# Kernel tuning notes

Measured on AMD Instinct MI355X. Metric: run time of the kernel, lower is better.

The kernel has to match this reference:

```python
import jax, jax.numpy as jnp
import numpy as np


def setup_inputs() -> dict:
    key = jax.random.key(0)
    k1, k2, k3 = jax.random.split(key, 3)
    B, L, S, H, E, D = 2, 512, 512, 8, 32, 64
    queries = jax.random.normal(k1, (B, L, H, E), dtype=jnp.float32)
    keys = jax.random.normal(k2, (B, S, H, E), dtype=jnp.float32)
    values = jax.random.normal(k3, (B, S, H, D), dtype=jnp.float32)
    v = jnp.ones((E,), dtype=jnp.float32)
    attn_mask_add = jnp.zeros((L, S), dtype=jnp.float32)
    key_lengths_add = jnp.zeros((B, S), dtype=jnp.float32)
    return {
        "queries": queries,
        "keys": keys,
        "values": values,
        "v": v,
        "attn_mask_add": attn_mask_add,
        "key_lengths_add": key_lengths_add,
    }


def reference(queries, keys, values, v, attn_mask_add, key_lengths_add):
    # Additive (Bahdanau) attention.
    # queries: (B,L,H,E), keys: (B,S,H,E), values: (B,S,H,D)
    # Broadcast add -> tanh -> contract with v: (B,L,S,H,E) -> (B,H,L,S)
    feat = jnp.tanh(queries[:, :, None, :, :] + keys[:, None, :, :, :])  # (B,L,S,H,E)
    scores = jnp.einsum("blshe,e->bhls", feat, v)  # (B,H,L,S)
    scores = scores + attn_mask_add[None, None, :, :]          # (L,S) attn mask
    scores = scores + key_lengths_add[:, None, None, :]        # (B,S) key-length mask
    A = jax.nn.softmax(scores, axis=-1)  # (B,H,L,S); dropout is identity (p=0 / eval)
    V = jnp.einsum("bhls,bshd->blhd", A, values)  # (B,L,H,D)
    return V
```

## Files before the change

kernel.cpp:

```cpp
#include <hip/hip_runtime.h>


#define BB 2
#define LL 512
#define SS 512
#define HH 8
#define EE 32
#define DD 64

#define WS_EK_OFF 0
#define WS_EQ_OFF (2u * 1024u * 1024u)
#define WS_VT_OFF (4u * 1024u * 1024u)
#define WS_PR_OFF (8u * 1024u * 1024u)
#define WS_SM_OFF (16u * 1024u * 1024u)

typedef __attribute__((ext_vector_type(8))) short bf16x8;
typedef __attribute__((ext_vector_type(4))) float f32x4;
typedef __attribute__((ext_vector_type(4))) unsigned u32x4;

__device__ __forceinline__ unsigned short f2bf(float f) {
    unsigned u = __float_as_uint(f);
    u += 0x7FFFu + ((u >> 16) & 1u);
    return (unsigned short)(u >> 16);
}
__device__ __forceinline__ float fast_exp2(float x) {
#if __has_builtin(__builtin_amdgcn_exp2f)
    return __builtin_amdgcn_exp2f(x);
#else
    return exp2f(x);
#endif
}
__device__ __forceinline__ float fast_rcp(float x) {
    return __builtin_amdgcn_rcpf(x);
}
__device__ __forceinline__ float bcastf(float x) {
    return __int_as_float(__builtin_amdgcn_readfirstlane(__float_as_int(x)));
}

#define SCV 2.885390081777927f

__global__ __launch_bounds__(256) void prep_kernel(
    const float* __restrict__ q, const float* __restrict__ k,
    const float* __restrict__ vals, float* __restrict__ ws)
{
    unsigned gid = blockIdx.x * 256 + threadIdx.x;
    if (gid < 32768u) {
        unsigned i  = gid;
        unsigned s  = i & 511u;
        unsigned e8 = (i >> 9) & 3u;
        unsigned h  = (i >> 11) & 7u;
        unsigned b  = i >> 14;
        const float* kr = k + (((size_t)b * SS + s) * HH + h) * EE + e8 * 8;
        float4 k0 = *(const float4*)kr;
        float4 k1 = *(const float4*)(kr + 4);
        u32x4 pk;
        pk[0] = (unsigned)f2bf(fast_exp2(SCV * k0.x)) |
                ((unsigned)f2bf(fast_exp2(SCV * k0.y)) << 16);
        pk[1] = (unsigned)f2bf(fast_exp2(SCV * k0.z)) |
                ((unsigned)f2bf(fast_exp2(SCV * k0.w)) << 16);
        pk[2] = (unsigned)f2bf(fast_exp2(SCV * k1.x)) |
                ((unsigned)f2bf(fast_exp2(SCV * k1.y)) << 16);
        pk[3] = (unsigned)f2bf(fast_exp2(SCV * k1.z)) |
                ((unsigned)f2bf(fast_exp2(SCV * k1.w)) << 16);
        ((u32x4*)((char*)ws + WS_EK_OFF))[i] = pk;
    } else if (gid < 98304u) {
        unsigned i = gid - 32768u;
        float4 qv = ((const float4*)q)[i];
        float4 ev = make_float4(fast_exp2(SCV * qv.x), fast_exp2(SCV * qv.y),
                                fast_exp2(SCV * qv.z), fast_exp2(SCV * qv.w));
        ((float4*)(ws + WS_EQ_OFF / 4))[i] = ev;
    } else {
        unsigned i      = gid - 98304u;
        unsigned lane   = i & 63u;
        unsigned c      = (i >> 6) & 15u;
        unsigned dchunk = (i >> 10) & 3u;
        unsigned h      = (i >> 12) & 7u;
        unsigned b      = i >> 15;
        unsigned qd = lane >> 4, n = lane & 15;
        unsigned d  = dchunk * 16 + n;
        unsigned s0 = c * 32 + qd * 8;
        const float* vb = vals + (((size_t)b * SS + s0) * HH + h) * DD + d;
        u32x4 pk;
        #pragma unroll
        for (int j2 = 0; j2 < 4; j2++) {
            float f0 = vb[(size_t)(2 * j2) * (HH * DD)];
            float f1 = vb[(size_t)(2 * j2 + 1) * (HH * DD)];
            pk[j2] = (unsigned)f2bf(f0) | ((unsigned)f2bf(f1) << 16);
        }
        ((u32x4*)((char*)ws + WS_VT_OFF))[i] = pk;
    }
}

__global__ __launch_bounds__(256) void score_kernel(
    const u32x4* __restrict__ ws_ekb,
    const float* __restrict__ ws_eqf,
    const float* __restrict__ vvec,
    const float* __restrict__ mask,
    const float* __restrict__ klen,
    unsigned short* __restrict__ ws_prob,
    float* __restrict__ ws_sum)
{
    __shared__ u32x4 sek[4 * SS];

    const int tid  = threadIdx.x;
    const int w    = tid >> 6;
    const int lane = tid & 63;
    const int bh   = blockIdx.x >> 6;
    const int lblk = blockIdx.x & 63;
    const int b    = bh >> 3;
    const int h    = bh & 7;
    const int lw   = lblk * 8 + 2 * w;

    {
        const u32x4* esrc = ws_ekb + (size_t)bh * (4 * SS);
        #pragma unroll
        for (int t = 0; t < 8; t++)
            sek[tid + t * 256] = esrc[tid + t * 256];
    }

    float eq0[EE], eq1[EE], v2s[EE];
    {
        const float* q0 = ws_eqf + (((size_t)b * LL + lw) * HH + h) * EE;
        const float* q1 = q0 + HH * EE;
        #pragma unroll
        for (int e = 0; e < EE; e += 4) {
            float4 t0 = *(const float4*)(q0 + e);
            float4 t1 = *(const float4*)(q1 + e);
            eq0[e] = bcastf(t0.x); eq0[e+1] = bcastf(t0.y);
            eq0[e+2] = bcastf(t0.z); eq0[e+3] = bcastf(t0.w);
            eq1[e] = bcastf(t1.x); eq1[e+1] = bcastf(t1.y);
            eq1[e+2] = bcastf(t1.z); eq1[e+3] = bcastf(t1.w);
        }
        const float4* vr = (const float4*)vvec;
        #pragma unroll
        for (int e4 = 0; e4 < EE / 4; e4++) {
            float4 t = vr[e4];
            v2s[e4*4]   = bcastf(-2.f * t.x); v2s[e4*4+1] = bcastf(-2.f * t.y);
            v2s[e4*4+2] = bcastf(-2.f * t.z); v2s[e4*4+3] = bcastf(-2.f * t.w);
        }
    }
    __syncthreads();

    float sc0[SS / 64], sc1[SS / 64];
    for (int i = 0; i < SS / 64; i++) {
        const int s = lane + i * 64;
        u32x4 g0 = sek[s];
        u32x4 g1 = sek[SS + s];
        u32x4 g2 = sek[2 * SS + s];
        u32x4 g3 = sek[3 * SS + s];
        float a0A = 0.f, a0B = 0.f, a1A = 0.f, a1B = 0.f;
        #define PAIR2(u, le, A0, A1)                                          \
        {                                                                     \
            float eklo = __uint_as_float((u) << 16);                          \
            float ekhi = __uint_as_float((u) & 0xffff0000u);                  \
            float qa0 = __builtin_fmaf(eq0[le], eklo, 1.f);                   \
            float qb0 = __builtin_fmaf(eq0[(le) + 1], ekhi, 1.f);             \
            float nm0 = __builtin_fmaf(v2s[le], qb0, v2s[(le) + 1] * qa0);    \
            A0 = __builtin_fmaf(nm0, fast_rcp(qa0 * qb0), A0);                \
            float qa1 = __builtin_fmaf(eq1[le], eklo, 1.f);                   \
            float qb1 = __builtin_fmaf(eq1[(le) + 1], ekhi, 1.f);             \
            float nm1 = __builtin_fmaf(v2s[le], qb1, v2s[(le) + 1] * qa1);    \
            A1 = __builtin_fmaf(nm1, fast_rcp(qa1 * qb1), A1);                \
        }
        PAIR2(g0[0], 0, a0A, a1A)  PAIR2(g0[1], 2, a0B, a1B)
        PAIR2(g0[2], 4, a0A, a1A)  PAIR2(g0[3], 6, a0B, a1B)
        PAIR2(g1[0], 8, a0A, a1A)  PAIR2(g1[1], 10, a0B, a1B)
        PAIR2(g1[2], 12, a0A, a1A) PAIR2(g1[3], 14, a0B, a1B)
        PAIR2(g2[0], 16, a0A, a1A) PAIR2(g2[1], 18, a0B, a1B)
        PAIR2(g2[2], 20, a0A, a1A) PAIR2(g2[3], 22, a0B, a1B)
        PAIR2(g3[0], 24, a0A, a1A) PAIR2(g3[1], 26, a0B, a1B)
        PAIR2(g3[2], 28, a0A, a1A) PAIR2(g3[3], 30, a0B, a1B)
        #undef PAIR2
        sc0[i] = a0A + a0B;
        sc1[i] = a1A + a1B;
    }

    {
        const float* kl = klen + (size_t)b * SS;
        float klv[SS / 64];
        #pragma unroll
        for (int i = 0; i < SS / 64; i++) klv[i] = kl[lane + i * 64];

        #pragma unroll
        for (int r = 0; r < 2; r++) {
            float* sc = r ? sc1 : sc0;
            const float* mrow = mask + (size_t)(lw + r) * SS;
            float ssum = 0.f;
            #pragma unroll
            for (int i = 0; i < SS / 64; i++) {
                float v = fminf(sc[i] + mrow[lane + i * 64] + klv[i], 80.f);
                sc[i] = __expf(v);
                ssum += sc[i];
            }
            #pragma unroll
            for (int off = 1; off < 64; off <<= 1) ssum += __shfl_xor(ssum, off, 64);
            unsigned short* pr = ws_prob + ((size_t)bh * LL + lw + r) * SS;
            #pragma unroll
            for (int i = 0; i < SS / 64; i++)
                pr[lane + i * 64] = f2bf(sc[i]);
            if (lane == 0) ws_sum[(size_t)bh * LL + lw + r] = ssum;
        }
    }
}

__global__ __launch_bounds__(256) void pv_kernel(
    const unsigned short* __restrict__ ws_prob,
    const float* __restrict__ ws_sum,
    const bf16x8* __restrict__ ws_vtf,
    float* __restrict__ out)
{
    const int tid  = threadIdx.x;
    const int w    = tid >> 6;
    const int lane = tid & 63;
    const int bh   = blockIdx.x >> 5;
    const int lt   = blockIdx.x & 31;
    const int b    = bh >> 3;
    const int h    = bh & 7;
    const int l0   = lt * 16;

    const int am = lane & 15;
    const int qd = lane >> 4;
    const unsigned short* ap = ws_prob + ((size_t)bh * LL + l0 + am) * SS + qd * 8;
    const bf16x8* vf = ws_vtf + ((size_t)(bh * 4 + w) * 16) * 64 + lane;

    f32x4 acc = {0.f, 0.f, 0.f, 0.f};
    bf16x8 af[4], bv[4];
    #pragma unroll
    for (int c = 0; c < 4; c++) {
        af[c] = *(const bf16x8*)(ap + c * 32);
        bv[c] = vf[c * 64];
    }
    #pragma unroll
    for (int c = 0; c < SS / 32; c++) {
        acc = __builtin_amdgcn_mfma_f32_16x16x32_bf16(af[c & 3], bv[c & 3],
                                                      acc, 0, 0, 0);
        if (c + 4 < SS / 32) {
            af[c & 3] = *(const bf16x8*)(ap + (c + 4) * 32);
            bv[c & 3] = vf[(c + 4) * 64];
        }
    }
    const int dof = w * 16 + am;
    float* orow = out + (((size_t)b * LL + l0 + qd * 4) * HH + h) * DD + dof;
    const float* sm = ws_sum + (size_t)bh * LL + l0 + qd * 4;
    #pragma unroll
    for (int r = 0; r < 4; r++)
        orow[(size_t)r * (HH * DD)] = acc[r] * fast_rcp(sm[r]);
}

extern "C" void kernel_launch(void* const* d_in, const int* in_sizes, int n_in,
                              void* d_out, int out_size, void* d_ws, size_t ws_size,
                              hipStream_t stream) {
    const float* q    = (const float*)d_in[0];
    const float* k    = (const float*)d_in[1];
    const float* vals = (const float*)d_in[2];
    const float* vvec = (const float*)d_in[3];
    const float* mask = (const float*)d_in[4];
    const float* klen = (const float*)d_in[5];
    float* outp = (float*)d_out;

    float* ws = (float*)d_ws;
    prep_kernel<<<dim3(640), dim3(256), 0, stream>>>(q, k, vals, ws);

    const u32x4* ws_ekb = (const u32x4*)((char*)d_ws + WS_EK_OFF);
    const float* ws_eqf = (const float*)((char*)d_ws + WS_EQ_OFF);
    const bf16x8* ws_vtf = (const bf16x8*)((char*)d_ws + WS_VT_OFF);
    unsigned short* ws_prob = (unsigned short*)((char*)d_ws + WS_PR_OFF);
    float* ws_sum = (float*)((char*)d_ws + WS_SM_OFF);

    score_kernel<<<dim3(BB * HH * (LL / 8)), dim3(256), 0, stream>>>(
        ws_ekb, ws_eqf, vvec, mask, klen, ws_prob, ws_sum);

    pv_kernel<<<dim3(BB * HH * (LL / 16)), dim3(256), 0, stream>>>(
        ws_prob, ws_sum, ws_vtf, outp);
}
```

Baseline: 108.1 us.

## Fuse score and PV kernels via LDS probability tile, compute exp(q) inline

```diff
diff --git a/kernel.cpp b/kernel.cpp
--- a/kernel.cpp
+++ b/kernel.cpp
@@ -9,10 +9,7 @@
 #define DD 64
 
 #define WS_EK_OFF 0
-#define WS_EQ_OFF (2u * 1024u * 1024u)
 #define WS_VT_OFF (4u * 1024u * 1024u)
-#define WS_PR_OFF (8u * 1024u * 1024u)
-#define WS_SM_OFF (16u * 1024u * 1024u)
 
 typedef __attribute__((ext_vector_type(8))) short bf16x8;
 typedef __attribute__((ext_vector_type(4))) float f32x4;
@@ -40,8 +37,8 @@
 #define SCV 2.885390081777927f
 
 __global__ __launch_bounds__(256) void prep_kernel(
-    const float* __restrict__ q, const float* __restrict__ k,
-    const float* __restrict__ vals, float* __restrict__ ws)
+    const float* __restrict__ k, const float* __restrict__ vals,
+    float* __restrict__ ws)
 {
     unsigned gid = blockIdx.x * 256 + threadIdx.x;
     if (gid < 32768u) {
@@ -63,14 +60,8 @@
         pk[3] = (unsigned)f2bf(fast_exp2(SCV * k1.z)) |
                 ((unsigned)f2bf(fast_exp2(SCV * k1.w)) << 16);
         ((u32x4*)((char*)ws + WS_EK_OFF))[i] = pk;
-    } else if (gid < 98304u) {
-        unsigned i = gid - 32768u;
-        float4 qv = ((const float4*)q)[i];
-        float4 ev = make_float4(fast_exp2(SCV * qv.x), fast_exp2(SCV * qv.y),
-                                fast_exp2(SCV * qv.z), fast_exp2(SCV * qv.w));
-        ((float4*)(ws + WS_EQ_OFF / 4))[i] = ev;
     } else {
-        unsigned i      = gid - 98304u;
+        unsigned i      = gid - 32768u;
         unsigned lane   = i & 63u;
         unsigned c      = (i >> 6) & 15u;
         unsigned dchunk = (i >> 10) & 3u;
@@ -91,16 +82,17 @@
     }
 }
 
-__global__ __launch_bounds__(256) void score_kernel(
+__global__ __launch_bounds__(256) void addattn_kernel(
     const u32x4* __restrict__ ws_ekb,
-    const float* __restrict__ ws_eqf,
+    const bf16x8* __restrict__ ws_vtf,
+    const float* __restrict__ q,
     const float* __restrict__ vvec,
     const float* __restrict__ mask,
     const float* __restrict__ klen,
-    unsigned short* __restrict__ ws_prob,
-    float* __restrict__ ws_sum)
+    float* __restrict__ out)
 {
     __shared__ u32x4 sek[4 * SS];
+    __shared__ unsigned short sAb[8][SS];
 
     const int tid  = threadIdx.x;
     const int w    = tid >> 6;
@@ -109,7 +101,8 @@
     const int lblk = blockIdx.x & 63;
     const int b    = bh >> 3;
     const int h    = bh & 7;
-    const int lw   = lblk * 8 + 2 * w;
+    const int l0   = lblk * 8;
+    const int lw   = l0 + 2 * w;
 
     {
         const u32x4* esrc = ws_ekb + (size_t)bh * (4 * SS);
@@ -120,16 +113,20 @@
 
     float eq0[EE], eq1[EE], v2s[EE];
     {
-        const float* q0 = ws_eqf + (((size_t)b * LL + lw) * HH + h) * EE;
+        const float* q0 = q + (((size_t)b * LL + lw) * HH + h) * EE;
         const float* q1 = q0 + HH * EE;
         #pragma unroll
         for (int e = 0; e < EE; e += 4) {
             float4 t0 = *(const float4*)(q0 + e);
             float4 t1 = *(const float4*)(q1 + e);
-            eq0[e] = bcastf(t0.x); eq0[e+1] = bcastf(t0.y);
-            eq0[e+2] = bcastf(t0.z); eq0[e+3] = bcastf(t0.w);
-            eq1[e] = bcastf(t1.x); eq1[e+1] = bcastf(t1.y);
-            eq1[e+2] = bcastf(t1.z); eq1[e+3] = bcastf(t1.w);
+            eq0[e]   = bcastf(fast_exp2(SCV * t0.x));
+            eq0[e+1] = bcastf(fast_exp2(SCV * t0.y));
+            eq0[e+2] = bcastf(fast_exp2(SCV * t0.z));
+            eq0[e+3] = bcastf(fast_exp2(SCV * t0.w));
+            eq1[e]   = bcastf(fast_exp2(SCV * t1.x));
+            eq1[e+1] = bcastf(fast_exp2(SCV * t1.y));
+            eq1[e+2] = bcastf(fast_exp2(SCV * t1.z));
+            eq1[e+3] = bcastf(fast_exp2(SCV * t1.w));
         }
         const float4* vr = (const float4*)vvec;
         #pragma unroll
@@ -194,57 +191,43 @@
             }
             #pragma unroll
             for (int off = 1; off < 64; off <<= 1) ssum += __shfl_xor(ssum, off, 64);
-            unsigned short* pr = ws_prob + ((size_t)bh * LL + lw + r) * SS;
+            float inv = fast_rcp(ssum);
+            const int row = 2 * w + r;
+            const int fsw = (row * 5) & 7;
             #pragma unroll
-            for (int i = 0; i < SS / 64; i++)
-                pr[lane + i * 64] = f2bf(sc[i]);
-            if (lane == 0) ws_sum[(size_t)bh * LL + lw + r] = ssum;
-        }
-    }
-}
-
-__global__ __launch_bounds__(256) void pv_kernel(
-    const unsigned short* __restrict__ ws_prob,
-    const float* __restrict__ ws_sum,
-    const bf16x8* __restrict__ ws_vtf,
-    float* __restrict__ out)
-{
-    const int tid  = threadIdx.x;
-    const int w    = tid >> 6;
-    const int lane = tid & 63;
-    const int bh   = blockIdx.x >> 5;
-    const int lt   = blockIdx.x & 31;
-    const int b    = bh >> 3;
-    const int h    = bh & 7;
-    const int l0   = lt * 16;
-
-    const int am = lane & 15;
-    const int qd = lane >> 4;
-    const unsigned short* ap = ws_prob + ((size_t)bh * LL + l0 + am) * SS + qd * 8;
-    const bf16x8* vf = ws_vtf + ((size_t)(bh * 4 + w) * 16) * 64 + lane;
-
+            for (int i = 0; i < SS / 64; i++) {
+                int col = lane + i * 64;
+                int pos = (((col >> 3) ^ fsw) << 3) | (col & 7);
+                sAb[row][pos] = f2bf(sc[i] * inv);
+            }
+        }
+    }
+    __syncthreads();
+
+    const int am  = lane & 15;
+    const int qd  = lane >> 4;
+    const int dof = w * 16 + am;
+    const int fam = (am * 5) & 7;
+    const bf16x8* vf =
+        ws_vtf + ((size_t)((b * HH + h) * 4 + w) * 16) * 64 + lane;
     f32x4 acc = {0.f, 0.f, 0.f, 0.f};
-    bf16x8 af[4], bv[4];
+    bf16x8 bv[4];
     #pragma unroll
-    for (int c = 0; c < 4; c++) {
-        af[c] = *(const bf16x8*)(ap + c * 32);
-        bv[c] = vf[c * 64];
-    }
+    for (int c = 0; c < 4; c++) bv[c] = vf[c * 64];
     #pragma unroll
     for (int c = 0; c < SS / 32; c++) {
-        acc = __builtin_amdgcn_mfma_f32_16x16x32_bf16(af[c & 3], bv[c & 3],
-                                                      acc, 0, 0, 0);
-        if (c + 4 < SS / 32) {
-            af[c & 3] = *(const bf16x8*)(ap + (c + 4) * 32);
-            bv[c & 3] = vf[(c + 4) * 64];
-        }
-    }
-    const int dof = w * 16 + am;
-    float* orow = out + (((size_t)b * LL + l0 + qd * 4) * HH + h) * DD + dof;
-    const float* sm = ws_sum + (size_t)bh * LL + l0 + qd * 4;
-    #pragma unroll
-    for (int r = 0; r < 4; r++)
-        orow[(size_t)r * (HH * DD)] = acc[r] * fast_rcp(sm[r]);
+        bf16x8 af = {0, 0, 0, 0, 0, 0, 0, 0};
+        if (am < 8)
+            af = *(const bf16x8*)&sAb[am][((c * 4 + qd) ^ fam) << 3];
+        acc = __builtin_amdgcn_mfma_f32_16x16x32_bf16(af, bv[c & 3], acc, 0, 0, 0);
+        if (c + 4 < SS / 32) bv[c & 3] = vf[(c + 4) * 64];
+    }
+    if (qd < 2) {
+        float* orow = out + (((size_t)b * LL + l0 + qd * 4) * HH + h) * DD + dof;
+        #pragma unroll
+        for (int r = 0; r < 4; r++)
+            orow[(size_t)r * (HH * DD)] = acc[r];
+    }
 }
 
 extern "C" void kernel_launch(void* const* d_in, const int* in_sizes, int n_in,
@@ -259,17 +242,10 @@
     float* outp = (float*)d_out;
 
     float* ws = (float*)d_ws;
-    prep_kernel<<<dim3(640), dim3(256), 0, stream>>>(q, k, vals, ws);
+    prep_kernel<<<dim3(384), dim3(256), 0, stream>>>(k, vals, ws);
 
     const u32x4* ws_ekb = (const u32x4*)((char*)d_ws + WS_EK_OFF);
-    const float* ws_eqf = (const float*)((char*)d_ws + WS_EQ_OFF);
     const bf16x8* ws_vtf = (const bf16x8*)((char*)d_ws + WS_VT_OFF);
-    unsigned short* ws_prob = (unsigned short*)((char*)d_ws + WS_PR_OFF);
-    float* ws_sum = (float*)((char*)d_ws + WS_SM_OFF);
-
-    score_kernel<<<dim3(BB * HH * (LL / 8)), dim3(256), 0, stream>>>(
-        ws_ekb, ws_eqf, vvec, mask, klen, ws_prob, ws_sum);
-
-    pv_kernel<<<dim3(BB * HH * (LL / 16)), dim3(256), 0, stream>>>(
-        ws_prob, ws_sum, ws_vtf, outp);
-}
+    addattn_kernel<<<dim3(BB * HH * (LL / 8)), dim3(256), 0, stream>>>(
+        ws_ekb, ws_vtf, q, vvec, mask, klen, outp);
+}
```

Result: faster. 92.96 us (median of 2 runs) (-14.0%).
